# Optimization experiments

Hardware: AMD Instinct MI355X
Metric: run time of the kernel (lower is better)

The kernel has to match this reference:

```python
import jax, jax.numpy as jnp
import numpy as np

B, S, E, H = 16, 1024, 320, 8
DH = E // H  # 40


def _lin(x, W, b):
    return x @ W.T + b


def setup_inputs() -> dict:
    key = jax.random.key(0)
    ks = jax.random.split(key, 16)

    def w(k, shape, fan_in):
        return jax.random.normal(k, shape, dtype=jnp.float32) / np.float32(np.sqrt(fan_in))

    z = lambda n: jnp.zeros((n,), jnp.float32)
    return {
        "sequence_features": jax.random.normal(ks[0], (B, S, E), dtype=jnp.float32),
        # feature_processor (shared, applied twice): Linear(320,320)+ReLU+Linear(320,320)
        "fpW1": w(ks[1], (E, E), E), "fpb1": z(E),
        "fpW2": w(ks[2], (E, E), E), "fpb2": z(E),
        # MultiheadAttention(320, 8) in/out projections
        "Wq": w(ks[3], (E, E), E), "bq": z(E),
        "Wk": w(ks[4], (E, E), E), "bk": z(E),
        "Wv": w(ks[5], (E, E), E), "bv": z(E),
        "Wo": w(ks[6], (E, E), E), "bo": z(E),
        # contact MLP: Linear(320,160)+ReLU+Linear(160,1)
        "mW1": w(ks[7], (160, E), E), "mb1": z(160),
        "mW2": w(ks[8], (1, 160), 160), "mb2": z(1),
        # position_predictor: Linear(640,320)+ReLU+Linear(320,160)+ReLU+Linear(160,3)
        "pW1": w(ks[9], (E, 2 * E), 2 * E), "pb1": z(E),
        "pW2": w(ks[10], (160, E), E), "pb2": z(160),
        "pW3": w(ks[11], (3, 160), 160), "pb3": z(3),
    }


def _forward(x, fpW1, fpb1, fpW2, fpb2, Wq, bq, Wk, bk, Wv, bv, Wo, bo,
             mW1, mb1, mW2, mb2, pW1, pb1, pW2, pb2, pW3, pb3):
    # feature_processor (dropout = identity in eval)
    backbone = _lin(jax.nn.relu(_lin(x, fpW1, fpb1)), fpW2, fpb2)        # [B,S,E]
    side = _lin(jax.nn.relu(_lin(backbone, fpW1, fpb1)), fpW2, fpb2)     # [B,S,E]

    # MultiheadAttention with batch_first=False semantics: input is treated as
    # [L=B, N=S, E], i.e. attention mixes over the batch axis (dim 0).
    q = _lin(x, Wq, bq).reshape(B, S, H, DH)
    k = _lin(x, Wk, bk).reshape(B, S, H, DH)
    v = _lin(x, Wv, bv).reshape(B, S, H, DH)
    scale = np.float32(1.0 / np.sqrt(DH))
    scores = jnp.einsum("lshd,mshd->shlm", q, k) * scale                 # [S,H,B,B]
    attn = jax.nn.softmax(scores, axis=-1)
    ctx = jnp.einsum("shlm,mshd->lshd", attn, v).reshape(B, S, E)
    attn_out = _lin(ctx, Wo, bo)                                         # [B,S,E]

    # per-position MLP -> scalar; torch broadcast-assigns it across the row
    prob = _lin(jax.nn.relu(_lin(attn_out, mW1, mb1)), mW2, mb2)         # [B,S,1]
    contact_map = jnp.broadcast_to(prob, (B, S, S))                      # [B,S,S]

    # refinement loop is a no-op: output == position_predictor(cat(bb, sc))
    comb = jnp.concatenate([backbone, side], axis=-1)                    # [B,S,640]
    h = jax.nn.relu(_lin(comb, pW1, pb1))
    h = jax.nn.relu(_lin(h, pW2, pb2))
    refined = _lin(h, pW3, pb3)                                          # [B,S,3]
    return backbone, side, contact_map, refined


def reference(sequence_features, fpW1, fpb1, fpW2, fpb2, Wq, bq, Wk, bk, Wv, bv,
              Wo, bo, mW1, mb1, mW2, mb2, pW1, pb1, pW2, pb2, pW3, pb3):
    return _forward(sequence_features, fpW1, fpb1, fpW2, fpb2, Wq, bq, Wk, bk,
                    Wv, bv, Wo, bo, mW1, mb1, mW2, mb2, pW1, pb1, pW2, pb2, pW3, pb3)
```

## Files before the change

### kernel.cpp

```cpp
#include <hip/hip_runtime.h>
#include <math.h>


#define M_ROWS 16384

typedef float f32x4 __attribute__((ext_vector_type(4)));
typedef __bf16 bf16x8 __attribute__((ext_vector_type(8)));
typedef unsigned short ushort_t;

typedef const __attribute__((address_space(1))) void* gas_ptr;
typedef __attribute__((address_space(3))) void* las_ptr;

__device__ __forceinline__ unsigned int f2bf(float f) {
    union { float f; unsigned int u; } v; v.f = f;
    unsigned int u = v.u + 0x7FFFu + ((v.u >> 16) & 1u);
    return u >> 16;
}
__device__ __forceinline__ float bf2f(ushort_t s) {
    union { unsigned int u; float f; } v; v.u = ((unsigned int)s) << 16;
    return v.f;
}

template<int BN>
__device__ __forceinline__ void gemm_core(
    int tx, int ty,
    const ushort_t* __restrict__ X1, const ushort_t* __restrict__ X2,
    int ksplit, int K, const ushort_t* __restrict__ W,
    char* smem, f32x4 (*acc)[2])
{
    constexpr int BM = 128, BK = 64;
    constexpr int WROWS = (BN == 64) ? 2 : 4;
    constexpr int WCOLS = 4 / WROWS;
    constexpr int WM = BM / WROWS;
    constexpr int WN = BN / WCOLS;
    constexpr int MF = WM / 16;
    constexpr int NF = WN / 16;

    ushort_t* As = (ushort_t*)smem;
    ushort_t* Bs = As + BM * BK;

    const int tid  = threadIdx.x;
    const int wave = tid >> 6;
    const int lane = tid & 63;
    const int m0 = ty * BM;
    const int n0 = tx * BN;
    const int wr = wave / WCOLS;
    const int wc = wave % WCOLS;
    const int sr = lane >> 3;
    const int su = lane & 7;

    for (int k0 = 0; k0 < K; k0 += BK) {
        #pragma unroll
        for (int i = 0; i < (BM * BK * 2) / 4096; ++i) {
            const int c = i * 4 + wave;
            const int r = c * 8 + sr;
            const int gk = k0 + (su ^ (r & 7)) * 8;
            const ushort_t* src;
            if (gk < ksplit) src = X1 + (size_t)(m0 + r) * ksplit + gk;
            else             src = X2 + (size_t)(m0 + r) * (K - ksplit) + (gk - ksplit);
            __builtin_amdgcn_global_load_lds((gas_ptr)src, (las_ptr)&As[c * 512], 16, 0, 0);
        }
        #pragma unroll
        for (int i = 0; i < (BN * BK * 2) / 4096; ++i) {
            const int c = i * 4 + wave;
            const int r = c * 8 + sr;
            const int gk = k0 + (su ^ (r & 7)) * 8;
            const ushort_t* src = W + (size_t)(n0 + r) * K + gk;
            __builtin_amdgcn_global_load_lds((gas_ptr)src, (las_ptr)&Bs[c * 512], 16, 0, 0);
        }
        __syncthreads();

        #pragma unroll
        for (int s = 0; s < 2; ++s) {
            bf16x8 a[MF], b[NF];
            #pragma unroll
            for (int mf = 0; mf < MF; ++mf) {
                const int r  = wr * WM + mf * 16 + (lane & 15);
                const int lu = (s * 4 + (lane >> 4)) ^ (r & 7);
                a[mf] = *reinterpret_cast<const bf16x8*>(&As[r * 64 + lu * 8]);
            }
            #pragma unroll
            for (int nf = 0; nf < NF; ++nf) {
                const int r  = wc * WN + nf * 16 + (lane & 15);
                const int lu = (s * 4 + (lane >> 4)) ^ (r & 7);
                b[nf] = *reinterpret_cast<const bf16x8*>(&Bs[r * 64 + lu * 8]);
            }
            #pragma unroll
            for (int mf = 0; mf < MF; ++mf)
                #pragma unroll
                for (int nf = 0; nf < NF; ++nf)
                    acc[mf][nf] = __builtin_amdgcn_mfma_f32_16x16x32_bf16(
                        a[mf], b[nf], acc[mf][nf], 0, 0, 0);
        }
        __syncthreads();
    }
}

template<int BN, bool RELU>
__device__ __forceinline__ void gemm_store(
    int tx, int ty, f32x4 (*acc)[2], const float* __restrict__ bias,
    float* __restrict__ outF, ushort_t* __restrict__ outB, int N)
{
    constexpr int WROWS = (BN == 64) ? 2 : 4;
    constexpr int WCOLS = 4 / WROWS;
    constexpr int WM = 128 / WROWS;
    constexpr int WN = BN / WCOLS;
    constexpr int MF = WM / 16;

    const int tid  = threadIdx.x;
    const int wave = tid >> 6;
    const int lane = tid & 63;
    const int wr = wave / WCOLS;
    const int wc = wave % WCOLS;

    #pragma unroll
    for (int nf = 0; nf < 2; ++nf) {
        const int gn = tx * BN + wc * WN + nf * 16 + (lane & 15);
        const float bv = bias[gn];
        #pragma unroll
        for (int mf = 0; mf < MF; ++mf) {
            #pragma unroll
            for (int i = 0; i < 4; ++i) {
                const int gm = ty * 128 + wr * WM + mf * 16 + (lane >> 4) * 4 + i;
                float v = acc[mf][nf][i] + bv;
                if (RELU) v = fmaxf(v, 0.f);
                if (outF) outF[(size_t)gm * N + gn] = v;
                if (outB) outB[(size_t)gm * N + gn] = (ushort_t)f2bf(v);
            }
        }
    }
}

template<int BN, bool RELU>
__device__ __forceinline__ void gemm_full_xy(
    int tx, int ty,
    const ushort_t* X1, const ushort_t* X2, int ksplit, int K,
    const ushort_t* W, const float* bias,
    float* outF, ushort_t* outB, int N, char* smem)
{
    constexpr int MF = (BN == 64) ? 4 : 2;
    f32x4 acc[MF][2];
    #pragma unroll
    for (int i = 0; i < MF; ++i) { acc[i][0] = (f32x4)0.f; acc[i][1] = (f32x4)0.f; }
    gemm_core<BN>(tx, ty, X1, X2, ksplit, K, W, smem, acc);
    gemm_store<BN, RELU>(tx, ty, acc, bias, outF, outB, N);
}

__device__ __forceinline__ void attn_dev(
    int ab, const ushort_t* __restrict__ qkv, ushort_t* __restrict__ ctx, char* smem)
{
    float* q_s = (float*)smem;
    float* k_s = q_s + 16 * 40;
    float* v_s = k_s + 16 * 40;
    float* p_s = v_s + 16 * 40;

    const int s   = ab >> 3;
    const int h   = ab & 7;
    const int tid = threadIdx.x;
    const int hb  = h * 40;

    if (tid < 240) {
        const int mat = tid / 80;
        const int rem = tid % 80;
        const int l = rem / 5, c8 = rem % 5;
        const size_t g = (size_t)(l * 1024 + s) * 960 + mat * 320 + hb + c8 * 8;
        bf16x8 vv = *reinterpret_cast<const bf16x8*>(&qkv[g]);
        const ushort_t* pu = reinterpret_cast<const ushort_t*>(&vv);
        float* dst = (mat == 0 ? q_s : mat == 1 ? k_s : v_s) + l * 40 + c8 * 8;
        #pragma unroll
        for (int j = 0; j < 8; ++j) dst[j] = bf2f(pu[j]);
    }
    __syncthreads();

    {
        const int l = tid >> 4, m = tid & 15;
        float sc = 0.f;
        #pragma unroll
        for (int d = 0; d < 40; ++d) sc += q_s[l * 40 + d] * k_s[m * 40 + d];
        sc *= 0.15811388300841897f;
        float mx = sc;
        #pragma unroll
        for (int off = 1; off < 16; off <<= 1) mx = fmaxf(mx, __shfl_xor(mx, off, 16));
        float e = expf(sc - mx);
        float sum = e;
        #pragma unroll
        for (int off = 1; off < 16; off <<= 1) sum += __shfl_xor(sum, off, 16);
        p_s[l * 16 + m] = e / sum;
    }
    __syncthreads();

    for (int idx = tid; idx < 16 * 40; idx += 256) {
        int l = idx / 40, d = idx % 40;
        float acc = 0.f;
        #pragma unroll
        for (int m = 0; m < 16; ++m) acc += p_s[l * 16 + m] * v_s[m * 40 + d];
        ctx[(size_t)(l * 1024 + s) * 320 + hb + d] = (ushort_t)f2bf(acc);
    }
}


__device__ __forceinline__ void stage64(
    const ushort_t* __restrict__ src, int row0, int ldk, int k0,
    ushort_t* dst, int wave, int sr, int su)
{
    #pragma unroll
    for (int i = 0; i < 2; ++i) {
        const int c = i * 4 + wave;
        const int r = c * 8 + sr;
        const int gk = k0 + (su ^ (r & 7)) * 8;
        __builtin_amdgcn_global_load_lds(
            (gas_ptr)(src + (size_t)(row0 + r) * ldk + gk),
            (las_ptr)&dst[c * 512], 16, 0, 0);
    }
}
__device__ __forceinline__ void stage32(
    const ushort_t* __restrict__ src, int row0, int ldk, int k0,
    ushort_t* dst, int wave, int sr, int su)
{
    const int r = wave * 8 + sr;
    const int gk = k0 + (su ^ (r & 7)) * 8;
    __builtin_amdgcn_global_load_lds(
        (gas_ptr)(src + (size_t)(row0 + r) * ldk + gk),
        (las_ptr)&dst[wave * 512], 16, 0, 0);
}

__device__ void fusedB32_dev(
    int panel, const ushort_t* __restrict__ bbB,
    const ushort_t* __restrict__ fpW1b, const float* __restrict__ fpb1,
    const ushort_t* __restrict__ fpW2b, const float* __restrict__ fpb2,
    float* __restrict__ out_side, ushort_t* __restrict__ sideB, char* smem)
{
    ushort_t* tpan = (ushort_t*)smem;
    ushort_t* As   = tpan + 5 * 2048;
    ushort_t* Bs   = As + 2048;

    const int tid = threadIdx.x, wave = tid >> 6, lane = tid & 63;
    const int row0 = panel * 32;
    const int wr = wave >> 1, wc = wave & 1;
    const int sr = lane >> 3, su = lane & 7;

    for (int nb = 0; nb < 5; ++nb) {
        f32x4 acc[2]; acc[0] = (f32x4)0.f; acc[1] = (f32x4)0.f;
        for (int k0 = 0; k0 < 320; k0 += 64) {
            stage32(bbB,   row0,    320, k0, As, wave, sr, su);
            stage64(fpW1b, nb * 64, 320, k0, Bs, wave, sr, su);
            __syncthreads();
            #pragma unroll
            for (int s = 0; s < 2; ++s) {
                bf16x8 a, b[2];
                {
                    const int r  = wr * 16 + (lane & 15);
                    const int lu = (s * 4 + (lane >> 4)) ^ (r & 7);
                    a = *reinterpret_cast<const bf16x8*>(&As[r * 64 + lu * 8]);
                }
                #pragma unroll
                for (int nf = 0; nf < 2; ++nf) {
                    const int r  = wc * 32 + nf * 16 + (lane & 15);
                    const int lu = (s * 4 + (lane >> 4)) ^ (r & 7);
                    b[nf] = *reinterpret_cast<const bf16x8*>(&Bs[r * 64 + lu * 8]);
                }
                #pragma unroll
                for (int nf = 0; nf < 2; ++nf)
                    acc[nf] = __builtin_amdgcn_mfma_f32_16x16x32_bf16(a, b[nf], acc[nf], 0, 0, 0);
            }
            __syncthreads();
        }
        #pragma unroll
        for (int nf = 0; nf < 2; ++nf) {
            const int col = wc * 32 + nf * 16 + (lane & 15);
            const float bv = fpb1[nb * 64 + col];
            #pragma unroll
            for (int i = 0; i < 4; ++i) {
                const int row = wr * 16 + (lane >> 4) * 4 + i;
                float v = fmaxf(acc[nf][i] + bv, 0.f);
                const int u = col >> 3;
                tpan[nb * 2048 + row * 64 + ((u ^ (row & 7)) * 8) + (col & 7)]
                    = (ushort_t)f2bf(v);
            }
        }
        __syncthreads();
    }

    for (int nb = 0; nb < 5; ++nb) {
        f32x4 acc[2]; acc[0] = (f32x4)0.f; acc[1] = (f32x4)0.f;
        for (int kt = 0; kt < 5; ++kt) {
            stage64(fpW2b, nb * 64, 320, kt * 64, Bs, wave, sr, su);
            __syncthreads();
            #pragma unroll
            for (int s = 0; s < 2; ++s) {
                bf16x8 a, b[2];
                {
                    const int r  = wr * 16 + (lane & 15);
                    const int lu = (s * 4 + (lane >> 4)) ^ (r & 7);
                    a = *reinterpret_cast<const bf16x8*>(&tpan[kt * 2048 + r * 64 + lu * 8]);
                }
                #pragma unroll
                for (int nf = 0; nf < 2; ++nf) {
                    const int r  = wc * 32 + nf * 16 + (lane & 15);
                    const int lu = (s * 4 + (lane >> 4)) ^ (r & 7);
                    b[nf] = *reinterpret_cast<const bf16x8*>(&Bs[r * 64 + lu * 8]);
                }
                #pragma unroll
                for (int nf = 0; nf < 2; ++nf)
                    acc[nf] = __builtin_amdgcn_mfma_f32_16x16x32_bf16(a, b[nf], acc[nf], 0, 0, 0);
            }
            __syncthreads();
        }
        #pragma unroll
        for (int nf = 0; nf < 2; ++nf) {
            const int gn = nb * 64 + wc * 32 + nf * 16 + (lane & 15);
            const float bv = fpb2[gn];
            #pragma unroll
            for (int i = 0; i < 4; ++i) {
                const int gm = row0 + wr * 16 + (lane >> 4) * 4 + i;
                float v = acc[nf][i] + bv;
                out_side[(size_t)gm * 320 + gn] = v;
                sideB[(size_t)gm * 320 + gn] = (ushort_t)f2bf(v);
            }
        }
    }
}

__device__ void fusedC32_dev(
    int panel, const ushort_t* __restrict__ bbB, const ushort_t* __restrict__ sideB,
    const ushort_t* __restrict__ pW1b, const float* __restrict__ pb1,
    const ushort_t* __restrict__ pW2b, const float* __restrict__ pb2,
    const float* __restrict__ pW3, const float* __restrict__ pb3,
    float* __restrict__ out_ref, char* smem)
{
    ushort_t* tpan = (ushort_t*)smem;
    ushort_t* As   = tpan + 5 * 2048;
    ushort_t* Bs   = As + 2048;
    float*    pSum = (float*)(Bs + 4096);

    const int tid = threadIdx.x, wave = tid >> 6, lane = tid & 63;
    const int row0 = panel * 32;
    const int wr = wave >> 1, wc = wave & 1;
    const int sr = lane >> 3, su = lane & 7;

    for (int nb = 0; nb < 5; ++nb) {
        f32x4 acc[2]; acc[0] = (f32x4)0.f; acc[1] = (f32x4)0.f;
        for (int k0 = 0; k0 < 640; k0 += 64) {
            {
                const int r = wave * 8 + sr;
                const int gk = k0 + (su ^ (r & 7)) * 8;
                const ushort_t* src = (gk < 320)
                    ? bbB   + (size_t)(row0 + r) * 320 + gk
                    : sideB + (size_t)(row0 + r) * 320 + (gk - 320);
                __builtin_amdgcn_global_load_lds((gas_ptr)src, (las_ptr)&As[wave * 512], 16, 0, 0);
            }
            stage64(pW1b, nb * 64, 640, k0, Bs, wave, sr, su);
            __syncthreads();
            #pragma unroll
            for (int s = 0; s < 2; ++s) {
                bf16x8 a, b[2];
                {
                    const int r  = wr * 16 + (lane & 15);
                    const int lu = (s * 4 + (lane >> 4)) ^ (r & 7);
                    a = *reinterpret_cast<const bf16x8*>(&As[r * 64 + lu * 8]);
                }
                #pragma unroll
                for (int nf = 0; nf < 2; ++nf) {
                    const int r  = wc * 32 + nf * 16 + (lane & 15);
                    const int lu = (s * 4 + (lane >> 4)) ^ (r & 7);
                    b[nf] = *reinterpret_cast<const bf16x8*>(&Bs[r * 64 + lu * 8]);
                }
                #pragma unroll
                for (int nf = 0; nf < 2; ++nf)
                    acc[nf] = __builtin_amdgcn_mfma_f32_16x16x32_bf16(a, b[nf], acc[nf], 0, 0, 0);
            }
            __syncthreads();
        }
        #pragma unroll
        for (int nf = 0; nf < 2; ++nf) {
            const int col = wc * 32 + nf * 16 + (lane & 15);
            const float bv = pb1[nb * 64 + col];
            #pragma unroll
            for (int i = 0; i < 4; ++i) {
                const int row = wr * 16 + (lane >> 4) * 4 + i;
                float v = fmaxf(acc[nf][i] + bv, 0.f);
                const int u = col >> 3;
                tpan[nb * 2048 + row * 64 + ((u ^ (row & 7)) * 8) + (col & 7)]
                    = (ushort_t)f2bf(v);
            }
        }
        __syncthreads();
    }

    float part[4][3];
    #pragma unroll
    for (int i = 0; i < 4; ++i) { part[i][0] = part[i][1] = part[i][2] = 0.f; }

    for (int ct = 0; ct < 5; ++ct) {
        f32x4 acc = (f32x4)0.f;
        for (int kt = 0; kt < 5; ++kt) {
            stage32(pW2b, ct * 32, 320, kt * 64, Bs, wave, sr, su);
            __syncthreads();
            #pragma unroll
            for (int s = 0; s < 2; ++s) {
                bf16x8 a, b;
                {
                    const int r  = wr * 16 + (lane & 15);
                    const int lu = (s * 4 + (lane >> 4)) ^ (r & 7);
                    a = *reinterpret_cast<const bf16x8*>(&tpan[kt * 2048 + r * 64 + lu * 8]);
                }
                {
                    const int r  = wc * 16 + (lane & 15);
                    const int lu = (s * 4 + (lane >> 4)) ^ (r & 7);
                    b = *reinterpret_cast<const bf16x8*>(&Bs[r * 64 + lu * 8]);
                }
                acc = __builtin_amdgcn_mfma_f32_16x16x32_bf16(a, b, acc, 0, 0, 0);
            }
            __syncthreads();
        }
        const int col = ct * 32 + wc * 16 + (lane & 15);
        const float bv = pb2[col];
        #pragma unroll
        for (int i = 0; i < 4; ++i) {
            float v = fmaxf(acc[i] + bv, 0.f);
            #pragma unroll
            for (int n = 0; n < 3; ++n)
                part[i][n] += v * pW3[n * 160 + col];
        }
    }
    #pragma unroll
    for (int off = 8; off; off >>= 1)
        #pragma unroll
        for (int i = 0; i < 4; ++i)
            #pragma unroll
            for (int n = 0; n < 3; ++n)
                part[i][n] += __shfl_xor(part[i][n], off, 16);
    if ((lane & 15) == 0) {
        #pragma unroll
        for (int i = 0; i < 4; ++i) {
            const int row = wr * 16 + (lane >> 4) * 4 + i;
            #pragma unroll
            for (int n = 0; n < 3; ++n)
                pSum[(wc * 32 + row) * 3 + n] = part[i][n];
        }
    }
    __syncthreads();
    if (tid < 96) {
        const int row = tid / 3, n = tid % 3;
        out_ref[(size_t)(row0 + row) * 3 + n] =
            pSum[row * 3 + n] + pSum[(32 + row) * 3 + n] + pb3[n];
    }
}

__device__ void fusedD_dev(
    int panel, const ushort_t* __restrict__ aoB,
    const ushort_t* __restrict__ mW1b, const float* __restrict__ mb1,
    const float* __restrict__ mW2, const float* __restrict__ mb2,
    float* __restrict__ out_cm, char* smem)
{
    ushort_t* As = (ushort_t*)smem;
    ushort_t* Bs = As + 4096;
    float* probs = (float*)(Bs + 2048);

    const int tid = threadIdx.x, wave = tid >> 6, lane = tid & 63;
    const int row0 = panel * 64;
    const int sr = lane >> 3, su = lane & 7;

    float part[4] = {0.f, 0.f, 0.f, 0.f};

    for (int ct = 0; ct < 5; ++ct) {
        f32x4 acc[2];
        acc[0] = acc[1] = (f32x4)0.f;
        for (int k0 = 0; k0 < 320; k0 += 64) {
            stage64(aoB,  row0,    320, k0, As, wave, sr, su);
            stage32(mW1b, ct * 32, 320, k0, Bs, wave, sr, su);
            __syncthreads();
            #pragma unroll
            for (int s = 0; s < 2; ++s) {
                bf16x8 a, b[2];
                {
                    const int r  = wave * 16 + (lane & 15);
                    const int lu = (s * 4 + (lane >> 4)) ^ (r & 7);
                    a = *reinterpret_cast<const bf16x8*>(&As[r * 64 + lu * 8]);
                }
                #pragma unroll
                for (int nf = 0; nf < 2; ++nf) {
                    const int r  = nf * 16 + (lane & 15);
                    const int lu = (s * 4 + (lane >> 4)) ^ (r & 7);
                    b[nf] = *reinterpret_cast<const bf16x8*>(&Bs[r * 64 + lu * 8]);
                }
                #pragma unroll
                for (int nf = 0; nf < 2; ++nf)
                    acc[nf] = __builtin_amdgcn_mfma_f32_16x16x32_bf16(a, b[nf], acc[nf], 0, 0, 0);
            }
            __syncthreads();
        }
        #pragma unroll
        for (int nf = 0; nf < 2; ++nf) {
            const int col = ct * 32 + nf * 16 + (lane & 15);
            const float bv = mb1[col];
            const float w  = mW2[col];
            #pragma unroll
            for (int i = 0; i < 4; ++i)
                part[i] += fmaxf(acc[nf][i] + bv, 0.f) * w;
        }
    }
    #pragma unroll
    for (int off = 8; off; off >>= 1)
        #pragma unroll
        for (int i = 0; i < 4; ++i)
            part[i] += __shfl_xor(part[i], off, 16);
    if ((lane & 15) == 0) {
        #pragma unroll
        for (int i = 0; i < 4; ++i)
            probs[wave * 16 + (lane >> 4) * 4 + i] = part[i] + mb2[0];
    }
    __syncthreads();

    for (int r = 0; r < 64; ++r) {
        const float p = probs[r];
        reinterpret_cast<float4*>(out_cm + (size_t)(row0 + r) * 1024)[tid] =
            make_float4(p, p, p, p);
    }
}


struct ConvDesc { const float* src; ushort_t* dst; };
struct ConvPack { ConvDesc d[5]; int start[6]; };

__device__ __forceinline__ void conv_unit(const ConvPack& p, int u, int tid)
{
    int i = 0;
    #pragma unroll
    for (int t = 0; t < 5; ++t) if (u >= p.start[t + 1]) i = t + 1;
    const int idx = ((u - p.start[i]) * 256 + tid) * 4;
    float4 v = *reinterpret_cast<const float4*>(&p.d[i].src[idx]);
    unsigned int lo = f2bf(v.x) | (f2bf(v.y) << 16);
    unsigned int hi = f2bf(v.z) | (f2bf(v.w) << 16);
    *reinterpret_cast<uint2*>(&p.d[i].dst[idx]) = make_uint2(lo, hi);
}

__global__ __launch_bounds__(256) void conv_k(ConvPack p)
{
    conv_unit(p, blockIdx.x, threadIdx.x);
}

__global__ __launch_bounds__(256) void k_g1(
    const ushort_t* __restrict__ xb, const ushort_t* __restrict__ Wcat,
    const float* __restrict__ fpb1, const float* __restrict__ bq,
    const float* __restrict__ bk, const float* __restrict__ bvv,
    ushort_t* __restrict__ t1b, ushort_t* __restrict__ qkvb, ConvPack cp)
{
    __shared__ __align__(16) char smem[24 * 1024];
    const int bid = blockIdx.x;
    if (bid >= 2560) { conv_unit(cp, bid - 2560, threadIdx.x); return; }

    const int xcd = bid & 7;
    const int i0  = bid >> 3;
    const int ty  = xcd * 16 + i0 / 20;
    const int tx  = i0 % 20;

    f32x4 acc[4][2];
    #pragma unroll
    for (int i = 0; i < 4; ++i) { acc[i][0] = (f32x4)0.f; acc[i][1] = (f32x4)0.f; }
    gemm_core<64>(tx, ty, xb, xb, 320, 320, Wcat, smem, acc);

    const int tid = threadIdx.x, wave = tid >> 6, lane = tid & 63;
    const int wr = wave >> 1, wc = wave & 1;
    #pragma unroll
    for (int nf = 0; nf < 2; ++nf) {
        const int gn = tx * 64 + wc * 32 + nf * 16 + (lane & 15);
        float bv;
        if      (gn < 320) bv = fpb1[gn];
        else if (gn < 640) bv = bq[gn - 320];
        else if (gn < 960) bv = bk[gn - 640];
        else               bv = bvv[gn - 960];
        #pragma unroll
        for (int mf = 0; mf < 4; ++mf) {
            #pragma unroll
            for (int i = 0; i < 4; ++i) {
                const int gm = ty * 128 + wr * 64 + mf * 16 + (lane >> 4) * 4 + i;
                float v = acc[mf][nf][i] + bv;
                if (gn < 320) t1b [(size_t)gm * 320 + gn] = (ushort_t)f2bf(fmaxf(v, 0.f));
                else          qkvb[(size_t)gm * 960 + gn - 320] = (ushort_t)f2bf(v);
            }
        }
    }
}

__global__ __launch_bounds__(256) void k_g2_attn(
    const ushort_t* __restrict__ t1b, const ushort_t* __restrict__ fpW2b,
    const float* __restrict__ fpb2, float* __restrict__ out_bb,
    ushort_t* __restrict__ bbB,
    const ushort_t* __restrict__ qkvb, ushort_t* __restrict__ ctxb)
{
    __shared__ __align__(16) char smem[24 * 1024];
    const int bid = blockIdx.x;
    if (bid < 640) {
        const int xcd = bid & 7, i0 = bid >> 3;
        const int ty = xcd * 16 + i0 / 5, tx = i0 % 5;
        gemm_full_xy<64, false>(tx, ty, t1b, t1b, 320, 320, fpW2b, fpb2, out_bb, bbB, 320, smem);
    } else {
        attn_dev(bid - 640, qkvb, ctxb, smem);
    }
}

__global__ __launch_bounds__(256) void k_l3(
    const ushort_t* __restrict__ bbB,
    const ushort_t* __restrict__ fpW1b, const float* __restrict__ fpb1,
    const ushort_t* __restrict__ fpW2b, const float* __restrict__ fpb2,
    float* __restrict__ out_side, ushort_t* __restrict__ sideB,
    const ushort_t* __restrict__ ctxb, const ushort_t* __restrict__ Wob,
    const float* __restrict__ bo, ushort_t* __restrict__ aoB)
{
    __shared__ __align__(16) char smem[32 * 1024];
    const int bid = blockIdx.x;
    if (bid < 512) {
        fusedB32_dev(bid, bbB, fpW1b, fpb1, fpW2b, fpb2, out_side, sideB, smem);
    } else {
        const int b = bid - 512;
        const int xcd = b & 7, i0 = b >> 3;
        const int ty = xcd * 16 + i0 / 5, tx = i0 % 5;
        gemm_full_xy<64, false>(tx, ty, ctxb, ctxb, 320, 320, Wob, bo, nullptr, aoB, 320, smem);
    }
}

__global__ __launch_bounds__(256) void k_l4(
    const ushort_t* __restrict__ bbB, const ushort_t* __restrict__ sideB,
    const ushort_t* __restrict__ pW1b, const float* __restrict__ pb1,
    const ushort_t* __restrict__ pW2b, const float* __restrict__ pb2,
    const float* __restrict__ pW3, const float* __restrict__ pb3,
    float* __restrict__ out_ref,
    const ushort_t* __restrict__ aoB,
    const ushort_t* __restrict__ mW1b, const float* __restrict__ mb1,
    const float* __restrict__ mW2, const float* __restrict__ mb2,
    float* __restrict__ out_cm)
{
    __shared__ __align__(16) char smem[34 * 1024];
    const int bid = blockIdx.x;
    if (bid < 512) fusedC32_dev(bid, bbB, sideB, pW1b, pb1, pW2b, pb2, pW3, pb3, out_ref, smem);
    else           fusedD_dev(bid - 512, aoB, mW1b, mb1, mW2, mb2, out_cm, smem);
}

extern "C" void kernel_launch(void* const* d_in, const int* in_sizes, int n_in,
                              void* d_out, int out_size, void* d_ws, size_t ws_size,
                              hipStream_t stream)
{
    const float* x    = (const float*)d_in[0];
    const float* fpW1 = (const float*)d_in[1];
    const float* fpb1 = (const float*)d_in[2];
    const float* fpW2 = (const float*)d_in[3];
    const float* fpb2 = (const float*)d_in[4];
    const float* Wq   = (const float*)d_in[5];
    const float* bq   = (const float*)d_in[6];
    const float* Wk   = (const float*)d_in[7];
    const float* bk   = (const float*)d_in[8];
    const float* Wv   = (const float*)d_in[9];
    const float* bv   = (const float*)d_in[10];
    const float* Wo   = (const float*)d_in[11];
    const float* bo   = (const float*)d_in[12];
    const float* mW1  = (const float*)d_in[13];
    const float* mb1  = (const float*)d_in[14];
    const float* mW2  = (const float*)d_in[15];
    const float* mb2  = (const float*)d_in[16];
    const float* pW1  = (const float*)d_in[17];
    const float* pb1  = (const float*)d_in[18];
    const float* pW2  = (const float*)d_in[19];
    const float* pb2  = (const float*)d_in[20];
    const float* pW3  = (const float*)d_in[21];
    const float* pb3  = (const float*)d_in[22];

    float* out      = (float*)d_out;
    float* out_bb   = out;
    float* out_side = out + 5242880;
    float* out_cm   = out + 2 * 5242880;
    float* out_ref  = out + 2 * 5242880 + 16777216;

    ushort_t* ws = (ushort_t*)d_ws;
    const size_t BUF = 5242880;
    ushort_t* xb    = ws;
    ushort_t* t1b   = ws + 1 * BUF;
    ushort_t* bbB   = ws + 2 * BUF;
    ushort_t* sideB = ws + 3 * BUF;
    ushort_t* qkvb  = ws + 4 * BUF;
    ushort_t* wb    = ws + 7 * BUF;
    ushort_t* fpW1b = wb;
    ushort_t* Wqb   = wb + 102400;
    ushort_t* Wkb   = wb + 204800;
    ushort_t* Wvb   = wb + 307200;
    ushort_t* fpW2b = wb + 409600;
    ushort_t* Wob   = wb + 512000;
    ushort_t* mW1b  = wb + 614400;
    ushort_t* pW1b  = wb + 665600;
    ushort_t* pW2b  = wb + 870400;

    ushort_t* ctxb = xb;
    ushort_t* aoB  = qkvb;

    dim3 blk(256);

    ConvPack cp0;
    {
        const float* s[5] = {x, fpW1, Wq, Wk, Wv};
        ushort_t*    d[5] = {xb, fpW1b, Wqb, Wkb, Wvb};
        const int    n[5] = {5120, 100, 100, 100, 100};
        int a = 0;
        for (int i = 0; i < 5; ++i) { cp0.d[i] = {s[i], d[i]}; cp0.start[i] = a; a += n[i]; }
        cp0.start[5] = a;
    }
    conv_k<<<dim3(5520), blk, 0, stream>>>(cp0);

    ConvPack cp1;
    {
        const float* s[5] = {fpW2, Wo, mW1, pW1, pW2};
        ushort_t*    d[5] = {fpW2b, Wob, mW1b, pW1b, pW2b};
        const int    n[5] = {100, 100, 50, 200, 50};
        int a = 0;
        for (int i = 0; i < 5; ++i) { cp1.d[i] = {s[i], d[i]}; cp1.start[i] = a; a += n[i]; }
        cp1.start[5] = a;
    }
    k_g1<<<dim3(2560 + 500), blk, 0, stream>>>(xb, wb, fpb1, bq, bk, bv, t1b, qkvb, cp1);

    k_g2_attn<<<dim3(8832), blk, 0, stream>>>(t1b, fpW2b, fpb2, out_bb, bbB, qkvb, ctxb);
    k_l3<<<dim3(1152), blk, 0, stream>>>(bbB, fpW1b, fpb1, fpW2b, fpb2,
                                         out_side, sideB, ctxb, Wob, bo, aoB);
    k_l4<<<dim3(768), blk, 0, stream>>>(bbB, sideB, pW1b, pb1, pW2b, pb2, pW3, pb3,
                                        out_ref, aoB, mW1b, mb1, mW2, mb2, out_cm);
}
```

Before: 148.7 us.

## Fuse backbone second GEMM into side panel kernel and Wo projection into contact MLP

Merges the backbone fpW2 GEMM into the per-32-row side-feature panel kernel, so each block computes backbone then side for its rows. It also fuses the attention output projection (Wo) into the contact-MLP panel, keeping the projected tile in LDS instead of writing aoB to global memory. This removes one kernel launch and a global round trip of intermediates. In exchange, the panel blocks each do more serial work with fewer blocks in flight, and the side-feature pass re-reads bbB that was just written by the same block.

Result: faster. 132.6 us (-10.8%).

```diff
diff --git a/kernel.cpp b/kernel.cpp
--- a/kernel.cpp
+++ b/kernel.cpp
@@ -96,56 +96,6 @@
     }
 }
 
-template<int BN, bool RELU>
-__device__ __forceinline__ void gemm_store(
-    int tx, int ty, f32x4 (*acc)[2], const float* __restrict__ bias,
-    float* __restrict__ outF, ushort_t* __restrict__ outB, int N)
-{
-    constexpr int WROWS = (BN == 64) ? 2 : 4;
-    constexpr int WCOLS = 4 / WROWS;
-    constexpr int WM = 128 / WROWS;
-    constexpr int WN = BN / WCOLS;
-    constexpr int MF = WM / 16;
-
-    const int tid  = threadIdx.x;
-    const int wave = tid >> 6;
-    const int lane = tid & 63;
-    const int wr = wave / WCOLS;
-    const int wc = wave % WCOLS;
-
-    #pragma unroll
-    for (int nf = 0; nf < 2; ++nf) {
-        const int gn = tx * BN + wc * WN + nf * 16 + (lane & 15);
-        const float bv = bias[gn];
-        #pragma unroll
-        for (int mf = 0; mf < MF; ++mf) {
-            #pragma unroll
-            for (int i = 0; i < 4; ++i) {
-                const int gm = ty * 128 + wr * WM + mf * 16 + (lane >> 4) * 4 + i;
-                float v = acc[mf][nf][i] + bv;
-                if (RELU) v = fmaxf(v, 0.f);
-                if (outF) outF[(size_t)gm * N + gn] = v;
-                if (outB) outB[(size_t)gm * N + gn] = (ushort_t)f2bf(v);
-            }
-        }
-    }
-}
-
-template<int BN, bool RELU>
-__device__ __forceinline__ void gemm_full_xy(
-    int tx, int ty,
-    const ushort_t* X1, const ushort_t* X2, int ksplit, int K,
-    const ushort_t* W, const float* bias,
-    float* outF, ushort_t* outB, int N, char* smem)
-{
-    constexpr int MF = (BN == 64) ? 4 : 2;
-    f32x4 acc[MF][2];
-    #pragma unroll
-    for (int i = 0; i < MF; ++i) { acc[i][0] = (f32x4)0.f; acc[i][1] = (f32x4)0.f; }
-    gemm_core<BN>(tx, ty, X1, X2, ksplit, K, W, smem, acc);
-    gemm_store<BN, RELU>(tx, ty, acc, bias, outF, outB, N);
-}
-
 __device__ __forceinline__ void attn_dev(
     int ab, const ushort_t* __restrict__ qkv, ushort_t* __restrict__ ctx, char* smem)
 {
@@ -224,10 +174,12 @@
         (las_ptr)&dst[wave * 512], 16, 0, 0);
 }
 
-__device__ void fusedB32_dev(
-    int panel, const ushort_t* __restrict__ bbB,
+
+__device__ void g2b_dev(
+    int panel, const ushort_t* __restrict__ t1b,
     const ushort_t* __restrict__ fpW1b, const float* __restrict__ fpb1,
     const ushort_t* __restrict__ fpW2b, const float* __restrict__ fpb2,
+    float* __restrict__ out_bb, ushort_t* __restrict__ bbB,
     float* __restrict__ out_side, ushort_t* __restrict__ sideB, char* smem)
 {
     ushort_t* tpan = (ushort_t*)smem;
@@ -238,6 +190,47 @@
     const int row0 = panel * 32;
     const int wr = wave >> 1, wc = wave & 1;
     const int sr = lane >> 3, su = lane & 7;
+
+    for (int nb = 0; nb < 5; ++nb) {
+        f32x4 acc[2]; acc[0] = (f32x4)0.f; acc[1] = (f32x4)0.f;
+        for (int k0 = 0; k0 < 320; k0 += 64) {
+            stage32(t1b,   row0,    320, k0, As, wave, sr, su);
+            stage64(fpW2b, nb * 64, 320, k0, Bs, wave, sr, su);
+            __syncthreads();
+            #pragma unroll
+            for (int s = 0; s < 2; ++s) {
+                bf16x8 a, b[2];
+                {
+                    const int r  = wr * 16 + (lane & 15);
+                    const int lu = (s * 4 + (lane >> 4)) ^ (r & 7);
+                    a = *reinterpret_cast<const bf16x8*>(&As[r * 64 + lu * 8]);
+                }
+                #pragma unroll
+                for (int nf = 0; nf < 2; ++nf) {
+                    const int r  = wc * 32 + nf * 16 + (lane & 15);
+                    const int lu = (s * 4 + (lane >> 4)) ^ (r & 7);
+                    b[nf] = *reinterpret_cast<const bf16x8*>(&Bs[r * 64 + lu * 8]);
+                }
+                #pragma unroll
+                for (int nf = 0; nf < 2; ++nf)
+                    acc[nf] = __builtin_amdgcn_mfma_f32_16x16x32_bf16(a, b[nf], acc[nf], 0, 0, 0);
+            }
+            __syncthreads();
+        }
+        #pragma unroll
+        for (int nf = 0; nf < 2; ++nf) {
+            const int gn = nb * 64 + wc * 32 + nf * 16 + (lane & 15);
+            const float bv = fpb2[gn];
+            #pragma unroll
+            for (int i = 0; i < 4; ++i) {
+                const int gm = row0 + wr * 16 + (lane >> 4) * 4 + i;
+                float v = acc[nf][i] + bv;
+                out_bb[(size_t)gm * 320 + gn] = v;
+                bbB[(size_t)gm * 320 + gn] = (ushort_t)f2bf(v);
+            }
+        }
+    }
+    __syncthreads();
 
     for (int nb = 0; nb < 5; ++nb) {
         f32x4 acc[2]; acc[0] = (f32x4)0.f; acc[1] = (f32x4)0.f;
@@ -447,40 +440,41 @@
     }
 }
 
-__device__ void fusedD_dev(
-    int panel, const ushort_t* __restrict__ aoB,
+__device__ void fusedD32_dev(
+    int panel, const ushort_t* __restrict__ ctxb,
+    const ushort_t* __restrict__ Wob, const float* __restrict__ bo,
     const ushort_t* __restrict__ mW1b, const float* __restrict__ mb1,
     const float* __restrict__ mW2, const float* __restrict__ mb2,
     float* __restrict__ out_cm, char* smem)
 {
-    ushort_t* As = (ushort_t*)smem;
-    ushort_t* Bs = As + 4096;
-    float* probs = (float*)(Bs + 2048);
+    ushort_t* tpan = (ushort_t*)smem;
+    ushort_t* As   = tpan + 5 * 2048;
+    ushort_t* Bs   = As + 2048;
+    float*    pSum = (float*)(Bs + 4096);
+    float*    probs= pSum + 64;
 
     const int tid = threadIdx.x, wave = tid >> 6, lane = tid & 63;
-    const int row0 = panel * 64;
+    const int row0 = panel * 32;
+    const int wr = wave >> 1, wc = wave & 1;
     const int sr = lane >> 3, su = lane & 7;
 
-    float part[4] = {0.f, 0.f, 0.f, 0.f};
-
-    for (int ct = 0; ct < 5; ++ct) {
-        f32x4 acc[2];
-        acc[0] = acc[1] = (f32x4)0.f;
+    for (int nb = 0; nb < 5; ++nb) {
+        f32x4 acc[2]; acc[0] = (f32x4)0.f; acc[1] = (f32x4)0.f;
         for (int k0 = 0; k0 < 320; k0 += 64) {
-            stage64(aoB,  row0,    320, k0, As, wave, sr, su);
-            stage32(mW1b, ct * 32, 320, k0, Bs, wave, sr, su);
+            stage32(ctxb, row0,    320, k0, As, wave, sr, su);
+            stage64(Wob,  nb * 64, 320, k0, Bs, wave, sr, su);
             __syncthreads();
             #pragma unroll
             for (int s = 0; s < 2; ++s) {
                 bf16x8 a, b[2];
                 {
-                    const int r  = wave * 16 + (lane & 15);
+                    const int r  = wr * 16 + (lane & 15);
                     const int lu = (s * 4 + (lane >> 4)) ^ (r & 7);
                     a = *reinterpret_cast<const bf16x8*>(&As[r * 64 + lu * 8]);
                 }
                 #pragma unroll
                 for (int nf = 0; nf < 2; ++nf) {
-                    const int r  = nf * 16 + (lane & 15);
+                    const int r  = wc * 32 + nf * 16 + (lane & 15);
                     const int lu = (s * 4 + (lane >> 4)) ^ (r & 7);
                     b[nf] = *reinterpret_cast<const bf16x8*>(&Bs[r * 64 + lu * 8]);
                 }
@@ -492,13 +486,49 @@
         }
         #pragma unroll
         for (int nf = 0; nf < 2; ++nf) {
-            const int col = ct * 32 + nf * 16 + (lane & 15);
-            const float bv = mb1[col];
-            const float w  = mW2[col];
-            #pragma unroll
-            for (int i = 0; i < 4; ++i)
-                part[i] += fmaxf(acc[nf][i] + bv, 0.f) * w;
-        }
+            const int col = wc * 32 + nf * 16 + (lane & 15);
+            const float bv = bo[nb * 64 + col];
+            #pragma unroll
+            for (int i = 0; i < 4; ++i) {
+                const int row = wr * 16 + (lane >> 4) * 4 + i;
+                float v = acc[nf][i] + bv;
+                const int u = col >> 3;
+                tpan[nb * 2048 + row * 64 + ((u ^ (row & 7)) * 8) + (col & 7)]
+                    = (ushort_t)f2bf(v);
+            }
+        }
+        __syncthreads();
+    }
+
+    float part[4] = {0.f, 0.f, 0.f, 0.f};
+    for (int ct = 0; ct < 5; ++ct) {
+        f32x4 acc = (f32x4)0.f;
+        for (int kt = 0; kt < 5; ++kt) {
+            stage32(mW1b, ct * 32, 320, kt * 64, Bs, wave, sr, su);
+            __syncthreads();
+            #pragma unroll
+            for (int s = 0; s < 2; ++s) {
+                bf16x8 a, b;
+                {
+                    const int r  = wr * 16 + (lane & 15);
+                    const int lu = (s * 4 + (lane >> 4)) ^ (r & 7);
+                    a = *reinterpret_cast<const bf16x8*>(&tpan[kt * 2048 + r * 64 + lu * 8]);
+                }
+                {
+                    const int r  = wc * 16 + (lane & 15);
+                    const int lu = (s * 4 + (lane >> 4)) ^ (r & 7);
+                    b = *reinterpret_cast<const bf16x8*>(&Bs[r * 64 + lu * 8]);
+                }
+                acc = __builtin_amdgcn_mfma_f32_16x16x32_bf16(a, b, acc, 0, 0, 0);
+            }
+            __syncthreads();
+        }
+        const int col = ct * 32 + wc * 16 + (lane & 15);
+        const float bv = mb1[col];
+        const float w  = mW2[col];
+        #pragma unroll
+        for (int i = 0; i < 4; ++i)
+            part[i] += fmaxf(acc[i] + bv, 0.f) * w;
     }
     #pragma unroll
     for (int off = 8; off; off >>= 1)
@@ -507,12 +537,16 @@
             part[i] += __shfl_xor(part[i], off, 16);
     if ((lane & 15) == 0) {
         #pragma unroll
-        for (int i = 0; i < 4; ++i)
-            probs[wave * 16 + (lane >> 4) * 4 + i] = part[i] + mb2[0];
+        for (int i = 0; i < 4; ++i) {
+            const int row = wr * 16 + (lane >> 4) * 4 + i;
+            pSum[wc * 32 + row] = part[i];
+        }
     }
     __syncthreads();
-
-    for (int r = 0; r < 64; ++r) {
+    if (tid < 32) probs[tid] = pSum[tid] + pSum[32 + tid] + mb2[0];
+    __syncthreads();
+
+    for (int r = 0; r < 32; ++r) {
         const float p = probs[r];
         reinterpret_cast<float4*>(out_cm + (size_t)(row0 + r) * 1024)[tid] =
             make_float4(p, p, p, p);
@@ -583,50 +617,29 @@
     }
 }
 
-__global__ __launch_bounds__(256) void k_g2_attn(
-    const ushort_t* __restrict__ t1b, const ushort_t* __restrict__ fpW2b,
-    const float* __restrict__ fpb2, float* __restrict__ out_bb,
-    ushort_t* __restrict__ bbB,
-    const ushort_t* __restrict__ qkvb, ushort_t* __restrict__ ctxb)
-{
-    __shared__ __align__(16) char smem[24 * 1024];
-    const int bid = blockIdx.x;
-    if (bid < 640) {
-        const int xcd = bid & 7, i0 = bid >> 3;
-        const int ty = xcd * 16 + i0 / 5, tx = i0 % 5;
-        gemm_full_xy<64, false>(tx, ty, t1b, t1b, 320, 320, fpW2b, fpb2, out_bb, bbB, 320, smem);
-    } else {
-        attn_dev(bid - 640, qkvb, ctxb, smem);
-    }
-}
-
-__global__ __launch_bounds__(256) void k_l3(
-    const ushort_t* __restrict__ bbB,
+__global__ __launch_bounds__(256) void k_l2(
+    const ushort_t* __restrict__ t1b,
     const ushort_t* __restrict__ fpW1b, const float* __restrict__ fpb1,
     const ushort_t* __restrict__ fpW2b, const float* __restrict__ fpb2,
+    float* __restrict__ out_bb, ushort_t* __restrict__ bbB,
     float* __restrict__ out_side, ushort_t* __restrict__ sideB,
-    const ushort_t* __restrict__ ctxb, const ushort_t* __restrict__ Wob,
-    const float* __restrict__ bo, ushort_t* __restrict__ aoB)
-{
-    __shared__ __align__(16) char smem[32 * 1024];
+    const ushort_t* __restrict__ qkvb, ushort_t* __restrict__ ctxb)
+{
+    __shared__ __align__(16) char smem[33 * 1024];
     const int bid = blockIdx.x;
-    if (bid < 512) {
-        fusedB32_dev(bid, bbB, fpW1b, fpb1, fpW2b, fpb2, out_side, sideB, smem);
-    } else {
-        const int b = bid - 512;
-        const int xcd = b & 7, i0 = b >> 3;
-        const int ty = xcd * 16 + i0 / 5, tx = i0 % 5;
-        gemm_full_xy<64, false>(tx, ty, ctxb, ctxb, 320, 320, Wob, bo, nullptr, aoB, 320, smem);
-    }
-}
-
-__global__ __launch_bounds__(256) void k_l4(
+    if (bid < 512) g2b_dev(bid, t1b, fpW1b, fpb1, fpW2b, fpb2,
+                           out_bb, bbB, out_side, sideB, smem);
+    else           attn_dev(bid - 512, qkvb, ctxb, smem);
+}
+
+__global__ __launch_bounds__(256) void k_l3(
     const ushort_t* __restrict__ bbB, const ushort_t* __restrict__ sideB,
     const ushort_t* __restrict__ pW1b, const float* __restrict__ pb1,
     const ushort_t* __restrict__ pW2b, const float* __restrict__ pb2,
     const float* __restrict__ pW3, const float* __restrict__ pb3,
     float* __restrict__ out_ref,
-    const ushort_t* __restrict__ aoB,
+    const ushort_t* __restrict__ ctxb,
+    const ushort_t* __restrict__ Wob, const float* __restrict__ bo,
     const ushort_t* __restrict__ mW1b, const float* __restrict__ mb1,
     const float* __restrict__ mW2, const float* __restrict__ mb2,
     float* __restrict__ out_cm)
@@ -634,7 +647,7 @@
     __shared__ __align__(16) char smem[34 * 1024];
     const int bid = blockIdx.x;
     if (bid < 512) fusedC32_dev(bid, bbB, sideB, pW1b, pb1, pW2b, pb2, pW3, pb3, out_ref, smem);
-    else           fusedD_dev(bid - 512, aoB, mW1b, mb1, mW2, mb2, out_cm, smem);
+    else           fusedD32_dev(bid - 512, ctxb, Wob, bo, mW1b, mb1, mW2, mb2, out_cm, smem);
 }
 
 extern "C" void kernel_launch(void* const* d_in, const int* in_sizes, int n_in,
@@ -690,7 +703,6 @@
     ushort_t* pW2b  = wb + 870400;
 
     ushort_t* ctxb = xb;
-    ushort_t* aoB  = qkvb;
 
     dim3 blk(256);
 
@@ -716,9 +728,8 @@
     }
     k_g1<<<dim3(2560 + 500), blk, 0, stream>>>(xb, wb, fpb1, bq, bk, bv, t1b, qkvb, cp1);
 
-    k_g2_attn<<<dim3(8832), blk, 0, stream>>>(t1b, fpW2b, fpb2, out_bb, bbB, qkvb, ctxb);
-    k_l3<<<dim3(1152), blk, 0, stream>>>(bbB, fpW1b, fpb1, fpW2b, fpb2,
-                                         out_side, sideB, ctxb, Wob, bo, aoB);
-    k_l4<<<dim3(768), blk, 0, stream>>>(bbB, sideB, pW1b, pb1, pW2b, pb2, pW3, pb3,
-                                        out_ref, aoB, mW1b, mb1, mW2, mb2, out_cm);
-}
+    k_l2<<<dim3(8704), blk, 0, stream>>>(t1b, fpW1b, fpb1, fpW2b, fpb2,
+                                         out_bb, bbB, out_side, sideB, qkvb, ctxb);
+    k_l3<<<dim3(1024), blk, 0, stream>>>(bbB, sideB, pW1b, pb1, pW2b, pb2, pW3, pb3,
+                                         out_ref, ctxb, Wob, bo, mW1b, mb1, mW2, mb2, out_cm);
+}
```
